# Performance work log

Hardware: AMD Instinct MI355X
Metric: run time of the kernel (lower is better)

## Reference

```python
import jax, jax.numpy as jnp
import numpy as np

D_MODEL = 1024
NUM_HEADS = 16
HEAD_DIM = D_MODEL // NUM_HEADS
B, S = 2, 2048


def setup_inputs() -> dict:
    key = jax.random.key(0)
    ks = jax.random.split(key, 16)
    sd = 1.0 / np.sqrt(D_MODEL)
    def lin(k):
        kw, kb = jax.random.split(k)
        W = jax.random.uniform(kw, (D_MODEL, D_MODEL), jnp.float32, -sd, sd)
        b = jax.random.uniform(kb, (D_MODEL,), jnp.float32, -sd, sd)
        return W, b
    Wq, bq = lin(ks[0]); Wk, bk = lin(ks[1]); Wv, bv = lin(ks[2]); Wo, bo = lin(ks[3])
    return {
        'q': jax.random.normal(ks[4], (B, S, D_MODEL), jnp.float32),
        'k': jax.random.normal(ks[5], (B, S, D_MODEL), jnp.float32),
        'v': jax.random.normal(ks[6], (B, S, D_MODEL), jnp.float32),
        'phase': jax.random.normal(ks[7], (B,), jnp.float32),
        'Wq': Wq, 'bq': bq, 'Wk': Wk, 'bk': bk, 'Wv': Wv, 'bv': bv, 'Wo': Wo, 'bo': bo,
        'phase_coupling': jnp.zeros((1, NUM_HEADS, 1, 1), jnp.float32),
        'attention_scale': jnp.ones((1,), jnp.float32),
        'stability_factor': jnp.ones((1,), jnp.float32),
    }


def reference(q, k, v, phase, Wq, bq, Wk, bk, Wv, bv, Wo, bo,
              phase_coupling, attention_scale, stability_factor):
    batch, seq, _ = q.shape
    scale = HEAD_DIM ** -0.5

    def split_heads(x):  # [B,S,D] -> [B,H,S,hd]
        return x.reshape(batch, -1, NUM_HEADS, HEAD_DIM).transpose(0, 2, 1, 3)

    qh = split_heads(q @ Wq.T + bq)
    kh = split_heads(k @ Wk.T + bk)
    vh = split_heads(v @ Wv.T + bv)

    scores = jnp.einsum('bhqd,bhkd->bhqk', qh, kh) * (scale * attention_scale)
    # phase modulation: phase [B] -> [B,1,1,1]; scores *= 1 + coupling*sin(phase)
    phase_factor = jnp.sin(phase)[:, None, None, None]
    scores = scores * (1.0 + phase_coupling * phase_factor)

    attn_weights = jax.nn.softmax(scores, axis=-1)  # dropout is identity in eval
    out = jnp.einsum('bhqk,bhkd->bhqd', attn_weights, vh)
    out = out.transpose(0, 2, 1, 3).reshape(batch, seq, D_MODEL)
    out = (out @ Wo.T + bo) * stability_factor
    return out, attn_weights
```

## Files before the change

### kernel.cpp

```cpp
#include <hip/hip_runtime.h>
#include <hip/hip_bf16.h>
#include <cstdint>
#include <cstddef>
#include <cmath>

#define NH 16
#define HD 64
#define SS 2048
#define DM 1024
#define MTOT 4096

typedef __attribute__((ext_vector_type(8))) short short8;
typedef __attribute__((ext_vector_type(4))) float float4v;
typedef __attribute__((ext_vector_type(4))) int int4v;
typedef __attribute__((ext_vector_type(4))) unsigned short ushort4v;

__device__ __forceinline__ unsigned short f2bf(float f){
  unsigned int u = __builtin_bit_cast(unsigned int, f);
  u += 0x7FFFu + ((u >> 16) & 1u);
  return (unsigned short)(u >> 16);
}

__device__ __forceinline__ void gload16(const void* g, void* l){
  __builtin_amdgcn_global_load_lds((const __attribute__((address_space(1))) void*)g,
                                   (__attribute__((address_space(3))) void*)l, 16, 0, 0);
}

__global__ __launch_bounds__(256) void cvt3_kernel(
    const float* __restrict__ s0, const float* __restrict__ s1, const float* __restrict__ s2,
    unsigned short* __restrict__ d0, unsigned short* __restrict__ d1, unsigned short* __restrict__ d2,
    int n){
  const int z = blockIdx.z;
  const float* src = z==0 ? s0 : (z==1 ? s1 : s2);
  unsigned short* dst = z==0 ? d0 : (z==1 ? d1 : d2);
  for (int i = (blockIdx.x*blockDim.x + threadIdx.x)*4; i < n; i += gridDim.x*blockDim.x*4){
    float4v v = *reinterpret_cast<const float4v*>(src + i);
    ushort4v o;
    o.x = f2bf(v.x); o.y = f2bf(v.y); o.z = f2bf(v.z); o.w = f2bf(v.w);
    *reinterpret_cast<ushort4v*>(dst + i) = o;
  }
}

__global__ __launch_bounds__(256) void cvt4_kernel(
    const float* __restrict__ s0, const float* __restrict__ s1,
    const float* __restrict__ s2, const float* __restrict__ s3,
    unsigned short* __restrict__ d0, unsigned short* __restrict__ d1,
    unsigned short* __restrict__ d2, unsigned short* __restrict__ d3,
    int n){
  const int z = blockIdx.z;
  const float* src = z==0 ? s0 : (z==1 ? s1 : (z==2 ? s2 : s3));
  unsigned short* dst = z==0 ? d0 : (z==1 ? d1 : (z==2 ? d2 : d3));
  for (int i = (blockIdx.x*blockDim.x + threadIdx.x)*4; i < n; i += gridDim.x*blockDim.x*4){
    float4v v = *reinterpret_cast<const float4v*>(src + i);
    ushort4v o;
    o.x = f2bf(v.x); o.y = f2bf(v.y); o.z = f2bf(v.z); o.w = f2bf(v.w);
    *reinterpret_cast<ushort4v*>(dst + i) = o;
  }
}

__global__ __launch_bounds__(256) void gemm_proj(
    const unsigned short* __restrict__ X0, const unsigned short* __restrict__ X1, const unsigned short* __restrict__ X2,
    const unsigned short* __restrict__ W0, const unsigned short* __restrict__ W1, const unsigned short* __restrict__ W2,
    const float* __restrict__ b0, const float* __restrict__ b1, const float* __restrict__ b2,
    unsigned short* __restrict__ O0, unsigned short* __restrict__ O1, unsigned short* __restrict__ O2){
  __shared__ unsigned short Alds[128*32];
  __shared__ unsigned short Blds[128*32];
  const int z = blockIdx.z;
  const unsigned short* A  = z==0 ? X0 : (z==1 ? X1 : X2);
  const unsigned short* Bw = z==0 ? W0 : (z==1 ? W1 : W2);
  const float* bias        = z==0 ? b0 : (z==1 ? b1 : b2);
  unsigned short* outp     = z==0 ? O0 : (z==1 ? O1 : O2);
  const bool vmode = (z == 2);
  const int K = DM;
  const int t = threadIdx.x;
  const int l = t & 63;
  const int w = t >> 6;
  const int m0 = blockIdx.y * 128, n0 = blockIdx.x * 128;
  const int wm = (w & 1)*64, wn = (w >> 1)*64;
  const int srow = t >> 2;
  const int scol = (t & 3)*8;
  const int lr = l & 15, lg = l >> 4;
  float4v acc[4][4] = {};
  for (int k0 = 0; k0 < K; k0 += 32){
    __syncthreads();
    gload16(A  + (size_t)(m0 + srow     )*K + k0 + scol, Alds + t*8);
    gload16(A  + (size_t)(m0 + srow + 64)*K + k0 + scol, Alds + 2048 + t*8);
    gload16(Bw + (size_t)(n0 + srow     )*K + k0 + scol, Blds + t*8);
    gload16(Bw + (size_t)(n0 + srow + 64)*K + k0 + scol, Blds + 2048 + t*8);
    asm volatile("s_waitcnt vmcnt(0)" ::: "memory");
    __syncthreads();
    short8 afrag[4], bfrag[4];
    #pragma unroll
    for (int mb = 0; mb < 4; ++mb)
      afrag[mb] = *reinterpret_cast<const short8*>(Alds + (wm + mb*16 + lr)*32 + lg*8);
    #pragma unroll
    for (int nb = 0; nb < 4; ++nb)
      bfrag[nb] = *reinterpret_cast<const short8*>(Blds + (wn + nb*16 + lr)*32 + lg*8);
    #pragma unroll
    for (int mb = 0; mb < 4; ++mb)
      #pragma unroll
      for (int nb = 0; nb < 4; ++nb)
        acc[mb][nb] = __builtin_amdgcn_mfma_f32_16x16x32_bf16(afrag[mb], bfrag[nb], acc[mb][nb], 0, 0, 0);
  }
  #pragma unroll
  for (int mb = 0; mb < 4; ++mb){
    #pragma unroll
    for (int nb = 0; nb < 4; ++nb){
      const int gn = n0 + wn + nb*16 + lr;
      const float biasv = bias[gn];
      #pragma unroll
      for (int r = 0; r < 4; ++r){
        const int gm = m0 + wm + mb*16 + lg*4 + r;
        float v = acc[mb][nb][r] + biasv;
        const int b_ = gm >> 11, s_ = gm & 2047, h_ = gn >> 6, d_ = gn & 63;
        if (!vmode)
          outp[((size_t)(b_*NH + h_)*SS + s_)*HD + d_] = f2bf(v);
        else
          outp[((size_t)(b_*NH + h_)*HD + d_)*SS + s_] = f2bf(v);
      }
    }
  }
}

__global__ __launch_bounds__(256) void gemm_out(const unsigned short* __restrict__ A,
                                                const unsigned short* __restrict__ Bw,
                                                const float* __restrict__ bias,
                                                float* __restrict__ outp,
                                                const float* __restrict__ oscale_p){
  __shared__ unsigned short Alds[128*32];
  __shared__ unsigned short Blds[128*32];
  const int K = DM, N = DM;
  const int t = threadIdx.x;
  const int l = t & 63;
  const int w = t >> 6;
  const int m0 = blockIdx.y * 128, n0 = blockIdx.x * 128;
  const int wm = (w & 1)*64, wn = (w >> 1)*64;
  const int srow = t >> 2;
  const int scol = (t & 3)*8;
  const int lr = l & 15, lg = l >> 4;
  float4v acc[4][4] = {};
  for (int k0 = 0; k0 < K; k0 += 32){
    __syncthreads();
    gload16(A  + (size_t)(m0 + srow     )*K + k0 + scol, Alds + t*8);
    gload16(A  + (size_t)(m0 + srow + 64)*K + k0 + scol, Alds + 2048 + t*8);
    gload16(Bw + (size_t)(n0 + srow     )*K + k0 + scol, Blds + t*8);
    gload16(Bw + (size_t)(n0 + srow + 64)*K + k0 + scol, Blds + 2048 + t*8);
    asm volatile("s_waitcnt vmcnt(0)" ::: "memory");
    __syncthreads();
    short8 afrag[4], bfrag[4];
    #pragma unroll
    for (int mb = 0; mb < 4; ++mb)
      afrag[mb] = *reinterpret_cast<const short8*>(Alds + (wm + mb*16 + lr)*32 + lg*8);
    #pragma unroll
    for (int nb = 0; nb < 4; ++nb)
      bfrag[nb] = *reinterpret_cast<const short8*>(Blds + (wn + nb*16 + lr)*32 + lg*8);
    #pragma unroll
    for (int mb = 0; mb < 4; ++mb)
      #pragma unroll
      for (int nb = 0; nb < 4; ++nb)
        acc[mb][nb] = __builtin_amdgcn_mfma_f32_16x16x32_bf16(afrag[mb], bfrag[nb], acc[mb][nb], 0, 0, 0);
  }
  const float osc = oscale_p[0];
  #pragma unroll
  for (int mb = 0; mb < 4; ++mb){
    #pragma unroll
    for (int nb = 0; nb < 4; ++nb){
      const int gn = n0 + wn + nb*16 + lr;
      const float biasv = bias[gn];
      #pragma unroll
      for (int r = 0; r < 4; ++r){
        const int gm = m0 + wm + mb*16 + lg*4 + r;
        outp[(size_t)gm*N + gn] = (acc[mb][nb][r] + biasv) * osc;
      }
    }
  }
}

__global__ __launch_bounds__(256, 4) void attn_kernel(
    const unsigned short* __restrict__ Qh,
    const unsigned short* __restrict__ Kh,
    const unsigned short* __restrict__ Vt,
    unsigned short* __restrict__ AO,
    float* __restrict__ attnW,
    const float* __restrict__ phase,
    const float* __restrict__ pc,
    const float* __restrict__ ascale)
{
  __shared__ float lred[4][32];
  __shared__ __attribute__((aligned(16))) float smem[32*260];

  const int t = threadIdx.x;
  const int w = t >> 6, l = t & 63;
  const int lr = l & 15, lg = l >> 4;
  const int bh = blockIdx.x, qt = blockIdx.y;
  const int b = bh >> 4, h = bh & 15;
  const int q0 = qt*32;
  const float scale2 = 0.125f * ascale[0] * (1.0f + pc[h] * sinf(phase[b]))
                       * 1.4426950408889634f;

  const unsigned short* qbase = Qh + ((size_t)bh*SS + q0 + lr)*HD + lg*8;
  short8 aq[2][2];
  aq[0][0] = *reinterpret_cast<const short8*>(qbase);
  aq[0][1] = *reinterpret_cast<const short8*>(qbase + 32);
  aq[1][0] = *reinterpret_cast<const short8*>(qbase + 16*HD);
  aq[1][1] = *reinterpret_cast<const short8*>(qbase + 16*HD + 32);

  const unsigned short* kbase1 = Kh + ((size_t)bh*SS + w*512 + lr)*HD + lg*8;
  float lsum[2] = {0.f, 0.f};
  #pragma unroll 2
  for (int tb = 0; tb < 32; ++tb){
    const unsigned short* kp = kbase1 + (size_t)tb*16*HD;
    short8 bk0 = *reinterpret_cast<const short8*>(kp);
    short8 bk1 = *reinterpret_cast<const short8*>(kp + 32);
    #pragma unroll
    for (int qs = 0; qs < 2; ++qs){
      float4v pacc = {};
      pacc = __builtin_amdgcn_mfma_f32_16x16x32_bf16(bk0, aq[qs][0], pacc, 0, 0, 0);
      pacc = __builtin_amdgcn_mfma_f32_16x16x32_bf16(bk1, aq[qs][1], pacc, 0, 0, 0);
      lsum[qs] += (exp2f(pacc[0]*scale2) + exp2f(pacc[1]*scale2))
                + (exp2f(pacc[2]*scale2) + exp2f(pacc[3]*scale2));
    }
  }
  #pragma unroll
  for (int mask = 16; mask < 64; mask <<= 1){
    lsum[0] += __shfl_xor(lsum[0], mask, 64);
    lsum[1] += __shfl_xor(lsum[1], mask, 64);
  }
  if (l < 16){
    lred[w][lr]    = lsum[0];
    lred[w][16+lr] = lsum[1];
  }
  __syncthreads();
  float cc[2];
  #pragma unroll
  for (int qs = 0; qs < 2; ++qs){
    const int row = qs*16 + lr;
    const float total = (lred[0][row] + lred[1][row]) + (lred[2][row] + lred[3][row]);
    cc[qs] = -__log2f(total);
  }

  float4v oacc[2][4] = {};
  float* gwb = attnW + ((size_t)bh*SS + q0)*SS;
  const unsigned short* kb2 = Kh + ((size_t)bh*SS + lr)*HD + lg*8;
  const unsigned short* vb2 = Vt + ((size_t)bh*HD + lr)*SS + lg*8;
  const int idxA = (((lg & 1)*2)*16 + lr)*4;
  const int idxB = idxA + 64;
  const bool hi = (lg >= 2);

  for (int ch = 0; ch < 8; ++ch){
    #pragma unroll
    for (int sub = 0; sub < 2; ++sub){
      const int tloc = ch*256 + w*64 + sub*32;
      const unsigned short* kp = kb2 + (size_t)tloc*HD;
      short8 k0A = *reinterpret_cast<const short8*>(kp);
      short8 k1A = *reinterpret_cast<const short8*>(kp + 32);
      short8 k0B = *reinterpret_cast<const short8*>(kp + 16*HD);
      short8 k1B = *reinterpret_cast<const short8*>(kp + 16*HD + 32);
      short8 bv[4];
      #pragma unroll
      for (int dt = 0; dt < 4; ++dt)
        bv[dt] = *reinterpret_cast<const short8*>(vb2 + (size_t)(dt*16)*SS + tloc);

      #pragma unroll
      for (int qs = 0; qs < 2; ++qs){
        float4v pA = {};
        pA = __builtin_amdgcn_mfma_f32_16x16x32_bf16(k0A, aq[qs][0], pA, 0, 0, 0);
        pA = __builtin_amdgcn_mfma_f32_16x16x32_bf16(k1A, aq[qs][1], pA, 0, 0, 0);
        float4v pB = {};
        pB = __builtin_amdgcn_mfma_f32_16x16x32_bf16(k0B, aq[qs][0], pB, 0, 0, 0);
        pB = __builtin_amdgcn_mfma_f32_16x16x32_bf16(k1B, aq[qs][1], pB, 0, 0, 0);
        float4v eA, eB;
        eA.x = exp2f(fmaf(pA[0], scale2, cc[qs]));
        eA.y = exp2f(fmaf(pA[1], scale2, cc[qs]));
        eA.z = exp2f(fmaf(pA[2], scale2, cc[qs]));
        eA.w = exp2f(fmaf(pA[3], scale2, cc[qs]));
        eB.x = exp2f(fmaf(pB[0], scale2, cc[qs]));
        eB.y = exp2f(fmaf(pB[1], scale2, cc[qs]));
        eB.z = exp2f(fmaf(pB[2], scale2, cc[qs]));
        eB.w = exp2f(fmaf(pB[3], scale2, cc[qs]));

        const int cw = w*64 + sub*32;
        *reinterpret_cast<float4v*>(&smem[(qs*16 + lr)*260 + cw + lg*4]) = eA;
        *reinterpret_cast<float4v*>(&smem[(qs*16 + lr)*260 + cw + 16 + lg*4]) = eB;

        const int w0A = ((int)f2bf(eA.y) << 16) | (int)f2bf(eA.x);
        const int w1A = ((int)f2bf(eA.w) << 16) | (int)f2bf(eA.z);
        const int w0B = ((int)f2bf(eB.y) << 16) | (int)f2bf(eB.x);
        const int w1B = ((int)f2bf(eB.w) << 16) | (int)f2bf(eB.z);
        const int a0 = __builtin_amdgcn_ds_bpermute(idxA, w0A);
        const int b0 = __builtin_amdgcn_ds_bpermute(idxA, w0B);
        const int a1 = __builtin_amdgcn_ds_bpermute(idxA, w1A);
        const int b1 = __builtin_amdgcn_ds_bpermute(idxA, w1B);
        const int a2 = __builtin_amdgcn_ds_bpermute(idxB, w0A);
        const int b2 = __builtin_amdgcn_ds_bpermute(idxB, w0B);
        const int a3 = __builtin_amdgcn_ds_bpermute(idxB, w1A);
        const int b3 = __builtin_amdgcn_ds_bpermute(idxB, w1B);
        int4v words;
        words.x = hi ? b0 : a0;
        words.y = hi ? b1 : a1;
        words.z = hi ? b2 : a2;
        words.w = hi ? b3 : a3;
        const short8 pa = __builtin_bit_cast(short8, words);
        #pragma unroll
        for (int dt = 0; dt < 4; ++dt)
          oacc[qs][dt] = __builtin_amdgcn_mfma_f32_16x16x32_bf16(pa, bv[dt], oacc[qs][dt], 0, 0, 0);
      }
    }
    __syncthreads();
    #pragma unroll
    for (int i = 0; i < 8; ++i){
      const int row = i*4 + w;
      const float4v val = *reinterpret_cast<const float4v*>(&smem[row*260 + l*4]);
      __builtin_nontemporal_store(val,
        reinterpret_cast<float4v*>(gwb + (size_t)row*SS + ch*256 + l*4));
    }
    __syncthreads();
  }

  float* ored = smem;
  #pragma unroll
  for (int c = 0; c < 2; ++c){
    if (c) __syncthreads();
    #pragma unroll
    for (int qs = 0; qs < 2; ++qs)
      #pragma unroll
      for (int dl = 0; dl < 2; ++dl)
        #pragma unroll
        for (int r = 0; r < 4; ++r)
          ored[w*1024 + (qs*16 + lg*4 + r)*32 + dl*16 + lr] = oacc[qs][c*2 + dl][r];
    __syncthreads();
    const int row = t >> 3, c4 = (t & 7);
    const float4v* o0 = reinterpret_cast<const float4v*>(smem);
    const int fi = row*8 + c4;
    float4v s = o0[fi];
    s += o0[fi + 256];
    s += o0[fi + 512];
    s += o0[fi + 768];
    ushort4v o4;
    o4.x = f2bf(s.x); o4.y = f2bf(s.y); o4.z = f2bf(s.z); o4.w = f2bf(s.w);
    *reinterpret_cast<ushort4v*>(AO + ((size_t)b*SS + q0 + row)*DM + h*HD + c*32 + c4*4) = o4;
  }
}

extern "C" void kernel_launch(void* const* d_in, const int* in_sizes, int n_in,
                              void* d_out, int out_size, void* d_ws, size_t ws_size,
                              hipStream_t stream){
  const float* q      = (const float*)d_in[0];
  const float* k      = (const float*)d_in[1];
  const float* v      = (const float*)d_in[2];
  const float* phase  = (const float*)d_in[3];
  const float* Wq     = (const float*)d_in[4];
  const float* bq     = (const float*)d_in[5];
  const float* Wk     = (const float*)d_in[6];
  const float* bk     = (const float*)d_in[7];
  const float* Wv     = (const float*)d_in[8];
  const float* bv     = (const float*)d_in[9];
  const float* Wo     = (const float*)d_in[10];
  const float* bo     = (const float*)d_in[11];
  const float* pc     = (const float*)d_in[12];
  const float* ascale = (const float*)d_in[13];
  const float* stab   = (const float*)d_in[14];

  unsigned short* Xq  = (unsigned short*)d_ws;
  unsigned short* Xk  = Xq  + 4194304;
  unsigned short* Xv  = Xk  + 4194304;
  unsigned short* Wqb = Xv  + 4194304;
  unsigned short* Wkb = Wqb + 1048576;
  unsigned short* Wvb = Wkb + 1048576;
  unsigned short* Wob = Wvb + 1048576;
  unsigned short* Qh  = Wob + 1048576;
  unsigned short* Kh  = Qh  + 4194304;
  unsigned short* Vt  = Kh  + 4194304;
  unsigned short* AO  = Vt  + 4194304;

  float* out0  = (float*)d_out;
  float* attnW = out0 + (size_t)MTOT*DM;

  cvt3_kernel<<<dim3(512,1,3), 256, 0, stream>>>(q, k, v, Xq, Xk, Xv, MTOT*DM);
  cvt4_kernel<<<dim3(128,1,4), 256, 0, stream>>>(Wq, Wk, Wv, Wo, Wqb, Wkb, Wvb, Wob, DM*DM);

  gemm_proj<<<dim3(DM/128, MTOT/128, 3), 256, 0, stream>>>(
      Xq, Xk, Xv, Wqb, Wkb, Wvb, bq, bk, bv, Qh, Kh, Vt);

  attn_kernel<<<dim3(32, SS/32, 1), 256, 0, stream>>>(Qh, Kh, Vt, AO, attnW,
                                                      phase, pc, ascale);

  gemm_out<<<dim3(DM/128, MTOT/128, 1), 256, 0, stream>>>(AO, Wob, bo, out0, stab);
}
```

Baseline: 288.9 us.

## Feed PV MFMA from shared-memory probabilities instead of bpermute shuffles

The P·V accumulation no longer repacks probabilities across lanes with ds_bpermute inside the QK loop. Each wave now reads the exp'd scores it already staged in shared memory for the attention-weights store, converts them to bf16 in MFMA A-operand layout, and runs the PV MFMAs after the chunk barrier. V loads are moved after the barrier as well. __syncthreads is replaced by a lighter barrier that waits only on LDS counters, so outstanding global stores are not drained. This restructures the inner schedule and adds LDS reads per chunk. It relies on the new barrier ordering being sufficient for correctness.

```diff
diff --git a/kernel.cpp b/kernel.cpp
--- a/kernel.cpp
+++ b/kernel.cpp
@@ -24,6 +24,12 @@
 __device__ __forceinline__ void gload16(const void* g, void* l){
   __builtin_amdgcn_global_load_lds((const __attribute__((address_space(1))) void*)g,
                                    (__attribute__((address_space(3))) void*)l, 16, 0, 0);
+}
+
+__device__ __forceinline__ void soft_barrier(){
+  asm volatile("s_waitcnt lgkmcnt(0)" ::: "memory");
+  __builtin_amdgcn_s_barrier();
+  __builtin_amdgcn_sched_barrier(0);
 }
 
 __global__ __launch_bounds__(256) void cvt3_kernel(
@@ -243,9 +249,6 @@
   float* gwb = attnW + ((size_t)bh*SS + q0)*SS;
   const unsigned short* kb2 = Kh + ((size_t)bh*SS + lr)*HD + lg*8;
   const unsigned short* vb2 = Vt + ((size_t)bh*HD + lr)*SS + lg*8;
-  const int idxA = (((lg & 1)*2)*16 + lr)*4;
-  const int idxB = idxA + 64;
-  const bool hi = (lg >= 2);
 
   for (int ch = 0; ch < 8; ++ch){
     #pragma unroll
@@ -256,11 +259,6 @@
       short8 k1A = *reinterpret_cast<const short8*>(kp + 32);
       short8 k0B = *reinterpret_cast<const short8*>(kp + 16*HD);
       short8 k1B = *reinterpret_cast<const short8*>(kp + 16*HD + 32);
-      short8 bv[4];
-      #pragma unroll
-      for (int dt = 0; dt < 4; ++dt)
-        bv[dt] = *reinterpret_cast<const short8*>(vb2 + (size_t)(dt*16)*SS + tloc);
-
       #pragma unroll
       for (int qs = 0; qs < 2; ++qs){
         float4v pA = {};
@@ -278,35 +276,21 @@
         eB.y = exp2f(fmaf(pB[1], scale2, cc[qs]));
         eB.z = exp2f(fmaf(pB[2], scale2, cc[qs]));
         eB.w = exp2f(fmaf(pB[3], scale2, cc[qs]));
-
         const int cw = w*64 + sub*32;
         *reinterpret_cast<float4v*>(&smem[(qs*16 + lr)*260 + cw + lg*4]) = eA;
         *reinterpret_cast<float4v*>(&smem[(qs*16 + lr)*260 + cw + 16 + lg*4]) = eB;
-
-        const int w0A = ((int)f2bf(eA.y) << 16) | (int)f2bf(eA.x);
-        const int w1A = ((int)f2bf(eA.w) << 16) | (int)f2bf(eA.z);
-        const int w0B = ((int)f2bf(eB.y) << 16) | (int)f2bf(eB.x);
-        const int w1B = ((int)f2bf(eB.w) << 16) | (int)f2bf(eB.z);
-        const int a0 = __builtin_amdgcn_ds_bpermute(idxA, w0A);
-        const int b0 = __builtin_amdgcn_ds_bpermute(idxA, w0B);
-        const int a1 = __builtin_amdgcn_ds_bpermute(idxA, w1A);
-        const int b1 = __builtin_amdgcn_ds_bpermute(idxA, w1B);
-        const int a2 = __builtin_amdgcn_ds_bpermute(idxB, w0A);
-        const int b2 = __builtin_amdgcn_ds_bpermute(idxB, w0B);
-        const int a3 = __builtin_amdgcn_ds_bpermute(idxB, w1A);
-        const int b3 = __builtin_amdgcn_ds_bpermute(idxB, w1B);
-        int4v words;
-        words.x = hi ? b0 : a0;
-        words.y = hi ? b1 : a1;
-        words.z = hi ? b2 : a2;
-        words.w = hi ? b3 : a3;
-        const short8 pa = __builtin_bit_cast(short8, words);
-        #pragma unroll
-        for (int dt = 0; dt < 4; ++dt)
-          oacc[qs][dt] = __builtin_amdgcn_mfma_f32_16x16x32_bf16(pa, bv[dt], oacc[qs][dt], 0, 0, 0);
       }
     }
-    __syncthreads();
+    soft_barrier();
+
+    short8 bv[2][4];
+    #pragma unroll
+    for (int sub = 0; sub < 2; ++sub)
+      #pragma unroll
+      for (int dt = 0; dt < 4; ++dt)
+        bv[sub][dt] = *reinterpret_cast<const short8*>(
+            vb2 + (size_t)(dt*16)*SS + ch*256 + w*64 + sub*32);
+
     #pragma unroll
     for (int i = 0; i < 8; ++i){
       const int row = i*4 + w;
@@ -314,7 +298,25 @@
       __builtin_nontemporal_store(val,
         reinterpret_cast<float4v*>(gwb + (size_t)row*SS + ch*256 + l*4));
     }
-    __syncthreads();
+
+    #pragma unroll
+    for (int qs = 0; qs < 2; ++qs){
+      #pragma unroll
+      for (int sub = 0; sub < 2; ++sub){
+        const int cw = w*64 + sub*32;
+        const float4v p0 = *reinterpret_cast<const float4v*>(&smem[(qs*16 + lr)*260 + cw + lg*8]);
+        const float4v p1 = *reinterpret_cast<const float4v*>(&smem[(qs*16 + lr)*260 + cw + lg*8 + 4]);
+        short8 pa;
+        pa[0]=(short)f2bf(p0.x); pa[1]=(short)f2bf(p0.y);
+        pa[2]=(short)f2bf(p0.z); pa[3]=(short)f2bf(p0.w);
+        pa[4]=(short)f2bf(p1.x); pa[5]=(short)f2bf(p1.y);
+        pa[6]=(short)f2bf(p1.z); pa[7]=(short)f2bf(p1.w);
+        #pragma unroll
+        for (int dt = 0; dt < 4; ++dt)
+          oacc[qs][dt] = __builtin_amdgcn_mfma_f32_16x16x32_bf16(pa, bv[sub][dt], oacc[qs][dt], 0, 0, 0);
+      }
+    }
+    soft_barrier();
   }
 
   float* ored = smem;
```

After: 289.8 us. About the same (+0.3%).

## Split attention into P·V kernel and separate attention-weight writer kernel

Applied to the files above, without the earlier changes.

Splits the fused attention kernel into two. attn_pv computes the row log-sum stats, saves them to workspace, and accumulates P·V over each wave's own key range, with higher occupancy (launch bounds 8). attnw_write recomputes QK^T using the saved stats and streams the normalized fp32 attention weights to global memory, replacing block barriers with a lighter lgkmcnt wait plus s_barrier. The aim is to decouple the write-bandwidth-bound weight output from the compute-bound P·V path, at the cost of recomputing QK^T and exp a third time and adding a launch.

```diff
diff --git a/kernel.cpp b/kernel.cpp
--- a/kernel.cpp
+++ b/kernel.cpp
@@ -24,6 +24,12 @@
 __device__ __forceinline__ void gload16(const void* g, void* l){
   __builtin_amdgcn_global_load_lds((const __attribute__((address_space(1))) void*)g,
                                    (__attribute__((address_space(3))) void*)l, 16, 0, 0);
+}
+
+__device__ __forceinline__ void soft_barrier(){
+  asm volatile("s_waitcnt lgkmcnt(0)" ::: "memory");
+  __builtin_amdgcn_s_barrier();
+  __builtin_amdgcn_sched_barrier(0);
 }
 
 __global__ __launch_bounds__(256) void cvt3_kernel(
@@ -176,18 +182,18 @@
   }
 }
 
-__global__ __launch_bounds__(256, 4) void attn_kernel(
+__global__ __launch_bounds__(256, 8) void attn_pv(
     const unsigned short* __restrict__ Qh,
     const unsigned short* __restrict__ Kh,
     const unsigned short* __restrict__ Vt,
     unsigned short* __restrict__ AO,
-    float* __restrict__ attnW,
+    float* __restrict__ stats,
     const float* __restrict__ phase,
     const float* __restrict__ pc,
     const float* __restrict__ ascale)
 {
   __shared__ float lred[4][32];
-  __shared__ __attribute__((aligned(16))) float smem[32*260];
+  __shared__ __attribute__((aligned(16))) float ored[4][32*32];
 
   const int t = threadIdx.x;
   const int w = t >> 6, l = t & 63;
@@ -205,11 +211,13 @@
   aq[1][0] = *reinterpret_cast<const short8*>(qbase + 16*HD);
   aq[1][1] = *reinterpret_cast<const short8*>(qbase + 16*HD + 32);
 
-  const unsigned short* kbase1 = Kh + ((size_t)bh*SS + w*512 + lr)*HD + lg*8;
+  const int tbase = w * 512;
+  const unsigned short* kbase = Kh + ((size_t)bh*SS + tbase + lr)*HD + lg*8;
+
   float lsum[2] = {0.f, 0.f};
   #pragma unroll 2
   for (int tb = 0; tb < 32; ++tb){
-    const unsigned short* kp = kbase1 + (size_t)tb*16*HD;
+    const unsigned short* kp = kbase + (size_t)tb*16*HD;
     short8 bk0 = *reinterpret_cast<const short8*>(kp);
     short8 bk1 = *reinterpret_cast<const short8*>(kp + 32);
     #pragma unroll
@@ -238,14 +246,129 @@
     const float total = (lred[0][row] + lred[1][row]) + (lred[2][row] + lred[3][row]);
     cc[qs] = -__log2f(total);
   }
+  if (w == 0 && l < 16){
+    stats[(size_t)bh*SS + q0 + lr]      = cc[0];
+    stats[(size_t)bh*SS + q0 + 16 + lr] = cc[1];
+  }
 
   float4v oacc[2][4] = {};
-  float* gwb = attnW + ((size_t)bh*SS + q0)*SS;
-  const unsigned short* kb2 = Kh + ((size_t)bh*SS + lr)*HD + lg*8;
-  const unsigned short* vb2 = Vt + ((size_t)bh*HD + lr)*SS + lg*8;
+  const unsigned short* vbase = Vt + ((size_t)bh*HD + lr)*SS + tbase + lg*8;
   const int idxA = (((lg & 1)*2)*16 + lr)*4;
   const int idxB = idxA + 64;
   const bool hi = (lg >= 2);
+
+  for (int tp = 0; tp < 16; ++tp){
+    const int tloc = tp*32;
+    const unsigned short* kpA = kbase + (size_t)tloc*HD;
+    short8 k0A = *reinterpret_cast<const short8*>(kpA);
+    short8 k1A = *reinterpret_cast<const short8*>(kpA + 32);
+    short8 k0B = *reinterpret_cast<const short8*>(kpA + 16*HD);
+    short8 k1B = *reinterpret_cast<const short8*>(kpA + 16*HD + 32);
+    short8 bv[4];
+    #pragma unroll
+    for (int dt = 0; dt < 4; ++dt)
+      bv[dt] = *reinterpret_cast<const short8*>(vbase + (size_t)(dt*16)*SS + tloc);
+
+    #pragma unroll
+    for (int qs = 0; qs < 2; ++qs){
+      float4v pA = {};
+      pA = __builtin_amdgcn_mfma_f32_16x16x32_bf16(k0A, aq[qs][0], pA, 0, 0, 0);
+      pA = __builtin_amdgcn_mfma_f32_16x16x32_bf16(k1A, aq[qs][1], pA, 0, 0, 0);
+      float4v pB = {};
+      pB = __builtin_amdgcn_mfma_f32_16x16x32_bf16(k0B, aq[qs][0], pB, 0, 0, 0);
+      pB = __builtin_amdgcn_mfma_f32_16x16x32_bf16(k1B, aq[qs][1], pB, 0, 0, 0);
+      float4v eA, eB;
+      eA.x = exp2f(fmaf(pA[0], scale2, cc[qs]));
+      eA.y = exp2f(fmaf(pA[1], scale2, cc[qs]));
+      eA.z = exp2f(fmaf(pA[2], scale2, cc[qs]));
+      eA.w = exp2f(fmaf(pA[3], scale2, cc[qs]));
+      eB.x = exp2f(fmaf(pB[0], scale2, cc[qs]));
+      eB.y = exp2f(fmaf(pB[1], scale2, cc[qs]));
+      eB.z = exp2f(fmaf(pB[2], scale2, cc[qs]));
+      eB.w = exp2f(fmaf(pB[3], scale2, cc[qs]));
+      const int w0A = ((int)f2bf(eA.y) << 16) | (int)f2bf(eA.x);
+      const int w1A = ((int)f2bf(eA.w) << 16) | (int)f2bf(eA.z);
+      const int w0B = ((int)f2bf(eB.y) << 16) | (int)f2bf(eB.x);
+      const int w1B = ((int)f2bf(eB.w) << 16) | (int)f2bf(eB.z);
+
+      const int a0 = __builtin_amdgcn_ds_bpermute(idxA, w0A);
+      const int b0 = __builtin_amdgcn_ds_bpermute(idxA, w0B);
+      const int a1 = __builtin_amdgcn_ds_bpermute(idxA, w1A);
+      const int b1 = __builtin_amdgcn_ds_bpermute(idxA, w1B);
+      const int a2 = __builtin_amdgcn_ds_bpermute(idxB, w0A);
+      const int b2 = __builtin_amdgcn_ds_bpermute(idxB, w0B);
+      const int a3 = __builtin_amdgcn_ds_bpermute(idxB, w1A);
+      const int b3 = __builtin_amdgcn_ds_bpermute(idxB, w1B);
+      int4v words;
+      words.x = hi ? b0 : a0;
+      words.y = hi ? b1 : a1;
+      words.z = hi ? b2 : a2;
+      words.w = hi ? b3 : a3;
+      const short8 pa = __builtin_bit_cast(short8, words);
+
+      #pragma unroll
+      for (int dt = 0; dt < 4; ++dt)
+        oacc[qs][dt] = __builtin_amdgcn_mfma_f32_16x16x32_bf16(pa, bv[dt], oacc[qs][dt], 0, 0, 0);
+    }
+  }
+
+  #pragma unroll
+  for (int c = 0; c < 2; ++c){
+    if (c) __syncthreads();
+    #pragma unroll
+    for (int qs = 0; qs < 2; ++qs)
+      #pragma unroll
+      for (int dl = 0; dl < 2; ++dl)
+        #pragma unroll
+        for (int r = 0; r < 4; ++r)
+          ored[w][(qs*16 + lg*4 + r)*32 + dl*16 + lr] = oacc[qs][c*2 + dl][r];
+    __syncthreads();
+    const int row = t >> 3, c4 = (t & 7);
+    const float4v* o0 = reinterpret_cast<const float4v*>(&ored[0][0]);
+    const int fi = row*8 + c4;
+    float4v s = o0[fi];
+    s += o0[fi + 256];
+    s += o0[fi + 512];
+    s += o0[fi + 768];
+    ushort4v o4;
+    o4.x = f2bf(s.x); o4.y = f2bf(s.y); o4.z = f2bf(s.z); o4.w = f2bf(s.w);
+    *reinterpret_cast<ushort4v*>(AO + ((size_t)b*SS + q0 + row)*DM + h*HD + c*32 + c4*4) = o4;
+  }
+}
+
+__global__ __launch_bounds__(256, 4) void attnw_write(
+    const unsigned short* __restrict__ Qh,
+    const unsigned short* __restrict__ Kh,
+    const float* __restrict__ stats,
+    float* __restrict__ attnW,
+    const float* __restrict__ phase,
+    const float* __restrict__ pc,
+    const float* __restrict__ ascale)
+{
+  __shared__ __attribute__((aligned(16))) float smem[32*260];
+
+  const int t = threadIdx.x;
+  const int w = t >> 6, l = t & 63;
+  const int lr = l & 15, lg = l >> 4;
+  const int qt = blockIdx.x, bh = blockIdx.y;
+  const int b = bh >> 4, h = bh & 15;
+  const int q0 = qt*32;
+  const float scale2 = 0.125f * ascale[0] * (1.0f + pc[h] * sinf(phase[b]))
+                       * 1.4426950408889634f;
+
+  const unsigned short* qbase = Qh + ((size_t)bh*SS + q0 + lr)*HD + lg*8;
+  short8 aq[2][2];
+  aq[0][0] = *reinterpret_cast<const short8*>(qbase);
+  aq[0][1] = *reinterpret_cast<const short8*>(qbase + 32);
+  aq[1][0] = *reinterpret_cast<const short8*>(qbase + 16*HD);
+  aq[1][1] = *reinterpret_cast<const short8*>(qbase + 16*HD + 32);
+
+  float cc[2];
+  cc[0] = stats[(size_t)bh*SS + q0 + lr];
+  cc[1] = stats[(size_t)bh*SS + q0 + 16 + lr];
+
+  float* gwb = attnW + ((size_t)bh*SS + q0)*SS;
+  const unsigned short* kb2 = Kh + ((size_t)bh*SS + lr)*HD + lg*8;
 
   for (int ch = 0; ch < 8; ++ch){
     #pragma unroll
@@ -256,11 +379,6 @@
       short8 k1A = *reinterpret_cast<const short8*>(kp + 32);
       short8 k0B = *reinterpret_cast<const short8*>(kp + 16*HD);
       short8 k1B = *reinterpret_cast<const short8*>(kp + 16*HD + 32);
-      short8 bv[4];
-      #pragma unroll
-      for (int dt = 0; dt < 4; ++dt)
-        bv[dt] = *reinterpret_cast<const short8*>(vb2 + (size_t)(dt*16)*SS + tloc);
-
       #pragma unroll
       for (int qs = 0; qs < 2; ++qs){
         float4v pA = {};
@@ -278,35 +396,12 @@
         eB.y = exp2f(fmaf(pB[1], scale2, cc[qs]));
         eB.z = exp2f(fmaf(pB[2], scale2, cc[qs]));
         eB.w = exp2f(fmaf(pB[3], scale2, cc[qs]));
-
         const int cw = w*64 + sub*32;
         *reinterpret_cast<float4v*>(&smem[(qs*16 + lr)*260 + cw + lg*4]) = eA;
         *reinterpret_cast<float4v*>(&smem[(qs*16 + lr)*260 + cw + 16 + lg*4]) = eB;
-
-        const int w0A = ((int)f2bf(eA.y) << 16) | (int)f2bf(eA.x);
-        const int w1A = ((int)f2bf(eA.w) << 16) | (int)f2bf(eA.z);
-        const int w0B = ((int)f2bf(eB.y) << 16) | (int)f2bf(eB.x);
-        const int w1B = ((int)f2bf(eB.w) << 16) | (int)f2bf(eB.z);
-        const int a0 = __builtin_amdgcn_ds_bpermute(idxA, w0A);
-        const int b0 = __builtin_amdgcn_ds_bpermute(idxA, w0B);
-        const int a1 = __builtin_amdgcn_ds_bpermute(idxA, w1A);
-        const int b1 = __builtin_amdgcn_ds_bpermute(idxA, w1B);
-        const int a2 = __builtin_amdgcn_ds_bpermute(idxB, w0A);
-        const int b2 = __builtin_amdgcn_ds_bpermute(idxB, w0B);
-        const int a3 = __builtin_amdgcn_ds_bpermute(idxB, w1A);
-        const int b3 = __builtin_amdgcn_ds_bpermute(idxB, w1B);
-        int4v words;
-        words.x = hi ? b0 : a0;
-        words.y = hi ? b1 : a1;
-        words.z = hi ? b2 : a2;
-        words.w = hi ? b3 : a3;
-        const short8 pa = __builtin_bit_cast(short8, words);
-        #pragma unroll
-        for (int dt = 0; dt < 4; ++dt)
-          oacc[qs][dt] = __builtin_amdgcn_mfma_f32_16x16x32_bf16(pa, bv[dt], oacc[qs][dt], 0, 0, 0);
       }
     }
-    __syncthreads();
+    soft_barrier();
     #pragma unroll
     for (int i = 0; i < 8; ++i){
       const int row = i*4 + w;
@@ -314,31 +409,7 @@
       __builtin_nontemporal_store(val,
         reinterpret_cast<float4v*>(gwb + (size_t)row*SS + ch*256 + l*4));
     }
-    __syncthreads();
-  }
-
-  float* ored = smem;
-  #pragma unroll
-  for (int c = 0; c < 2; ++c){
-    if (c) __syncthreads();
-    #pragma unroll
-    for (int qs = 0; qs < 2; ++qs)
-      #pragma unroll
-      for (int dl = 0; dl < 2; ++dl)
-        #pragma unroll
-        for (int r = 0; r < 4; ++r)
-          ored[w*1024 + (qs*16 + lg*4 + r)*32 + dl*16 + lr] = oacc[qs][c*2 + dl][r];
-    __syncthreads();
-    const int row = t >> 3, c4 = (t & 7);
-    const float4v* o0 = reinterpret_cast<const float4v*>(smem);
-    const int fi = row*8 + c4;
-    float4v s = o0[fi];
-    s += o0[fi + 256];
-    s += o0[fi + 512];
-    s += o0[fi + 768];
-    ushort4v o4;
-    o4.x = f2bf(s.x); o4.y = f2bf(s.y); o4.z = f2bf(s.z); o4.w = f2bf(s.w);
-    *reinterpret_cast<ushort4v*>(AO + ((size_t)b*SS + q0 + row)*DM + h*HD + c*32 + c4*4) = o4;
+    soft_barrier();
   }
 }
 
@@ -372,6 +443,7 @@
   unsigned short* Kh  = Qh  + 4194304;
   unsigned short* Vt  = Kh  + 4194304;
   unsigned short* AO  = Vt  + 4194304;
+  float* stats = (float*)(AO + 4194304);
 
   float* out0  = (float*)d_out;
   float* attnW = out0 + (size_t)MTOT*DM;
@@ -382,7 +454,10 @@
   gemm_proj<<<dim3(DM/128, MTOT/128, 3), 256, 0, stream>>>(
       Xq, Xk, Xv, Wqb, Wkb, Wvb, bq, bk, bv, Qh, Kh, Vt);
 
-  attn_kernel<<<dim3(32, SS/32, 1), 256, 0, stream>>>(Qh, Kh, Vt, AO, attnW,
+  attn_pv<<<dim3(32, SS/32, 1), 256, 0, stream>>>(Qh, Kh, Vt, AO, stats,
+                                                  phase, pc, ascale);
+
+  attnw_write<<<dim3(SS/32, 32, 1), 256, 0, stream>>>(Qh, Kh, stats, attnW,
                                                       phase, pc, ascale);
 
   gemm_out<<<dim3(DM/128, MTOT/128, 1), 256, 0, stream>>>(AO, Wob, bo, out0, stab);
```

Result: slower. 528.2 us (+82.8%).
